# Kernel optimization log

Measured on AMD Instinct MI355X. Metric: run time of the kernel, lower is better.

## Reference

```python
import jax, jax.numpy as jnp
import numpy as np

IN_MODES = (4, 4, 6, 8)  # prod = 768 = d_model; same modes for input and output
D_MODEL = 768
N_HEADS = 12
D_HEAD = D_MODEL // N_HEADS
SCALE = 1.0 / np.sqrt(D_HEAD)
TT_RANKS = (1, 32, 64, 32, 1)


def tt_linear(x, c0, c1, c2, c3, b):
    # TT-factorized linear: cores c_k have shape (r_{k-1}, m_k, n_k, r_k)
    # with in/out modes IN_MODES. x: [B, S, 768]
    B, S, D = x.shape
    t = x.reshape(B * S, *IN_MODES)                     # n i j k l over in-modes
    t = jnp.einsum('nijkl,mir->njklmr', t, c0[0])       # contract n1, r0=1 squeezed
    t = jnp.einsum('njklmr,rpjs->nklmps', t, c1)        # contract n2 and rank r1
    t = jnp.einsum('nklmps,sqkt->nlmpqt', t, c2)        # contract n3 and rank r2
    t = jnp.einsum('nlmpqt,tul->nmpqu', t, c3[..., 0])  # contract n4 and rank r3, r4=1
    return t.reshape(B, S, D) + b                        # out-modes m,p,q,u -> 768


def _make_tt_params(key):
    ks = jax.random.split(key, 4)
    cores = []
    for i in range(4):
        shape = (TT_RANKS[i], IN_MODES[i], IN_MODES[i], TT_RANKS[i + 1])
        cores.append(jax.random.normal(ks[i], shape, jnp.float32) * 0.05)
    bias = jnp.zeros((D_MODEL,), jnp.float32)
    return cores, bias


def setup_inputs() -> dict:
    key = jax.random.key(0)
    kx, kq, kk, kv, ko = jax.random.split(key, 5)
    B, S = 2, 2048
    x = jax.random.normal(kx, (B, S, D_MODEL), jnp.float32)
    mask = jnp.tril(jnp.ones((S, S), dtype=bool))[None, None]  # causal [1,1,S,S]
    out = {'x': x, 'mask': mask}
    for name, k in (('q', kq), ('k', kk), ('v', kv), ('o', ko)):
        cores, bias = _make_tt_params(k)
        for i in range(4):
            out[f'{name}c{i}'] = cores[i]
        out[f'{name}b'] = bias
    return out


def reference(x, mask,
              qc0, qc1, qc2, qc3, qb,
              kc0, kc1, kc2, kc3, kb,
              vc0, vc1, vc2, vc3, vb,
              oc0, oc1, oc2, oc3, ob):
    B, S, _ = x.shape
    q = tt_linear(x, qc0, qc1, qc2, qc3, qb)
    k = tt_linear(x, kc0, kc1, kc2, kc3, kb)
    v = tt_linear(x, vc0, vc1, vc2, vc3, vb)
    # [B, S, H, Dh] -> [B, H, S, Dh]
    q = q.reshape(B, S, N_HEADS, D_HEAD).transpose(0, 2, 1, 3)
    k = k.reshape(B, S, N_HEADS, D_HEAD).transpose(0, 2, 1, 3)
    v = v.reshape(B, S, N_HEADS, D_HEAD).transpose(0, 2, 1, 3)
    scores = jnp.einsum('bhqd,bhkd->bhqk', q, k) * SCALE  # full O(S^2) scores
    scores = jnp.where(mask, scores, jnp.float32(-10000.0))  # masked_fill(mask==0,-1e4)
    attn = jax.nn.softmax(scores, axis=-1)  # dropout is identity at eval
    out = jnp.einsum('bhqk,bhkd->bhqd', attn, v)
    out = out.transpose(0, 2, 1, 3).reshape(B, S, D_MODEL)
    return tt_linear(out, oc0, oc1, oc2, oc3, ob)
```

## Files before the change

kernel.cpp:

```cpp
#include <hip/hip_runtime.h>
#include <cstddef>
#include <cstdint>

#define D_MODEL 768
#define N_HEADS 12
#define SEQ 2048
#define BATCH 2
#define NROWS (BATCH * SEQ)
#define W_ELEMS (D_MODEL * D_MODEL)
#define Y_ELEMS (NROWS * D_MODEL)

typedef __attribute__((ext_vector_type(8))) short bf16x8;
typedef __attribute__((ext_vector_type(4))) float f32x4;

struct TTPtrs {
    const float* c0[4];
    const float* c1[4];
    const float* c2[4];
    const float* c3[4];
};

__device__ __forceinline__ float bf2f(uint16_t u) {
    union { uint32_t u; float f; } c; c.u = ((uint32_t)u) << 16; return c.f;
}
__device__ __forceinline__ uint16_t f2bf(float f) {
    union { float f; uint32_t u; } c; c.f = f;
    uint32_t x = c.u + 0x7fffu + ((c.u >> 16) & 1u);
    return (uint16_t)(x >> 16);
}
__device__ __forceinline__ uint32_t cvtpk(float lo, float hi) {
    uint32_t r;
    asm("v_cvt_pk_bf16_f32 %0, %1, %2" : "=v"(r) : "v"(lo), "v"(hi));
    return r;
}
__device__ __forceinline__ void glds16(const void* g, void* l) {
    auto gp = reinterpret_cast<const __attribute__((address_space(1))) uint32_t*>(
        reinterpret_cast<uintptr_t>(g));
    auto lp = reinterpret_cast<__attribute__((address_space(3))) uint32_t*>(
        reinterpret_cast<uintptr_t>(l));
    __builtin_amdgcn_global_load_lds(gp, lp, 16, 0, 0);
}

__global__ __launch_bounds__(256) void pre_kernel(TTPtrs P, float* __restrict__ wsA,
                                                  const float* __restrict__ x,
                                                  uint16_t* __restrict__ xb) {
    const int bx = blockIdx.x;
    if (bx < 256) {
        const int mat = bx >> 6;
        const float* c0 = P.c0[mat];
        const float* c1 = P.c1[mat];
        float* A = wsA + mat * 16384;
        int idx = (bx & 63) * 256 + threadIdx.x;
        int s = idx & 63, pj = (idx >> 6) & 15, mi = idx >> 10;
        float acc = 0.f;
        #pragma unroll 8
        for (int r = 0; r < 32; r++)
            acc = fmaf(c0[mi * 32 + r], c1[(r * 16 + pj) * 64 + s], acc);
        A[idx] = acc;
    } else {
        int idx = ((bx - 256) * 256 + threadIdx.x) * 4;
        float4 v = *(const float4*)(x + idx);
        *(uint2*)(xb + idx) = make_uint2(cvtpk(v.x, v.y), cvtpk(v.z, v.w));
    }
}

__global__ __launch_bounds__(256) void tt_buildB(TTPtrs P, const float* __restrict__ wsA,
                                                 float* __restrict__ wsB) {
    const int mat = blockIdx.y;
    const float* c2 = P.c2[mat];
    const float* A = wsA + mat * 16384;
    float* B = wsB + (size_t)mat * 294912;
    int idx = blockIdx.x * 256 + threadIdx.x;
    int t = idx & 31;
    int rest = idx >> 5;
    int qk = rest % 36;
    int rest2 = rest / 36;
    int pj = rest2 & 15, mi = rest2 >> 4;
    const float* Arow = A + (mi * 16 + pj) * 64;
    float acc = 0.f;
    #pragma unroll 8
    for (int s = 0; s < 64; s++)
        acc = fmaf(Arow[s], c2[(s * 36 + qk) * 32 + t], acc);
    B[idx] = acc;
}

__global__ __launch_bounds__(256) void tt_buildC(TTPtrs P, const float* __restrict__ wsB,
                                                 uint16_t* __restrict__ Wbf) {
    __shared__ float b_lds[36 * 33];
    __shared__ float c_lds[32 * 64];
    const int mat = blockIdx.y;
    const int mipj = blockIdx.x;
    const int mi = mipj >> 4, pj = mipj & 15;
    const int m = mi >> 2, i = mi & 3, p = pj >> 2, j = pj & 3;
    const float* Bsrc = wsB + (size_t)mat * 294912 + (size_t)mipj * 1152;
    const float* c3 = P.c3[mat];
    uint16_t* Wt = Wbf + (size_t)mat * W_ELEMS;
    const int tid = threadIdx.x;

    for (int e = tid; e < 1152; e += 256) {
        int qk = e >> 5, t = e & 31;
        b_lds[qk * 33 + t] = Bsrc[e];
    }
    for (int e = tid; e < 2048; e += 256)
        c_lds[e] = c3[e];
    __syncthreads();

    const int outbase = (m * 4 + p) * 48;
    const int inbase = (i * 4 + j) * 48;
    #pragma unroll
    for (int n = 0; n < 9; n++) {
        int idx = n * 256 + tid;
        int qu = idx / 48, kl = idx % 48;
        int q = qu >> 3, u = qu & 7, k = kl >> 3, l = kl & 7;
        const float* brow = &b_lds[(q * 6 + k) * 33];
        const float* crow = &c_lds[u * 8 + l];
        float acc = 0.f;
        #pragma unroll 8
        for (int t = 0; t < 32; t++)
            acc = fmaf(brow[t], crow[t * 64], acc);
        Wt[(size_t)(outbase + qu) * D_MODEL + inbase + kl] = f2bf(acc);
    }
}

template <int MODE>
__global__ __launch_bounds__(256) void gemm_mfma(const uint16_t* __restrict__ X,
                                                 const uint16_t* __restrict__ Wall,
                                                 const float* __restrict__ b0,
                                                 const float* __restrict__ b1,
                                                 const float* __restrict__ b2,
                                                 void* __restrict__ Yall,
                                                 uint16_t* __restrict__ Vt) {
    __shared__ uint16_t lds[2][8192];
    const int z = blockIdx.z;
    const uint16_t* W = Wall + (size_t)z * W_ELEMS;
    const float* bias = (z == 0) ? b0 : (z == 1 ? b1 : b2);
    const int m0 = blockIdx.x * 128, n0 = blockIdx.y * 128;
    const int tid = threadIdx.x, w = tid >> 6, l = tid & 63;
    const int wr = w >> 1, wc = w & 1;
    const int l15 = l & 15, lg = l >> 4;

    const int srow = w * 32 + (l >> 2);
    const int scol = ((l & 3) ^ ((l >> 2) & 3)) * 8;
    const uint16_t* Abase = X + (size_t)(m0 + srow) * D_MODEL + scol;
    const uint16_t* Bbase = W + (size_t)(n0 + srow) * D_MODEL + scol;

    f32x4 acc[4][4];
    #pragma unroll
    for (int mi = 0; mi < 4; ++mi)
        #pragma unroll
        for (int ni = 0; ni < 4; ++ni) acc[mi][ni] = (f32x4){0.f, 0.f, 0.f, 0.f};

    auto stage = [&](int buf, int kt) {
        const uint16_t* A0 = Abase + kt * 32;
        const uint16_t* B0 = Bbase + kt * 32;
        glds16(A0, &lds[buf][w * 1024]);
        glds16(A0 + 16 * D_MODEL, &lds[buf][w * 1024 + 512]);
        glds16(B0, &lds[buf][4096 + w * 1024]);
        glds16(B0 + 16 * D_MODEL, &lds[buf][4096 + w * 1024 + 512]);
    };

    stage(0, 0);
    __syncthreads();
    const int roff = ((lg ^ (l & 3)) << 3);
    for (int kt = 0; kt < 24; ++kt) {
        int cur = kt & 1;
        if (kt < 23) stage(cur ^ 1, kt + 1);
        const uint16_t* As = &lds[cur][0];
        const uint16_t* Bs = &lds[cur][4096];
        bf16x8 a[4], bb[4];
        #pragma unroll
        for (int mi = 0; mi < 4; ++mi)
            a[mi] = *(const bf16x8*)(As + (wr * 64 + mi * 16 + l15) * 32 + roff);
        #pragma unroll
        for (int ni = 0; ni < 4; ++ni)
            bb[ni] = *(const bf16x8*)(Bs + (wc * 64 + ni * 16 + l15) * 32 + roff);
        #pragma unroll
        for (int mi = 0; mi < 4; ++mi)
            #pragma unroll
            for (int ni = 0; ni < 4; ++ni)
                acc[mi][ni] = __builtin_amdgcn_mfma_f32_16x16x32_bf16(
                    a[mi], bb[ni], acc[mi][ni], 0, 0, 0);
        __syncthreads();
    }

    float bv[4];
    #pragma unroll
    for (int ni = 0; ni < 4; ++ni) bv[ni] = bias[n0 + wc * 64 + ni * 16 + l15];

    if (MODE == 1 && z == 2) {
        #pragma unroll
        for (int mi = 0; mi < 4; ++mi) {
            int row = m0 + wr * 64 + mi * 16 + lg * 4;
            int bb_ = row >> 11, s = row & 2047;
            #pragma unroll
            for (int ni = 0; ni < 4; ++ni) {
                int col = n0 + wc * 64 + ni * 16 + l15;
                float v0 = acc[mi][ni][0] + bv[ni], v1 = acc[mi][ni][1] + bv[ni];
                float v2 = acc[mi][ni][2] + bv[ni], v3 = acc[mi][ni][3] + bv[ni];
                *(uint2*)(Vt + ((size_t)(bb_ * 12 + (col >> 6)) * 64 + (col & 63)) * 2048 + s) =
                    make_uint2(cvtpk(v0, v1), cvtpk(v2, v3));
            }
        }
    } else {
        #pragma unroll
        for (int mi = 0; mi < 4; ++mi)
            #pragma unroll
            for (int ni = 0; ni < 4; ++ni)
                #pragma unroll
                for (int r = 0; r < 4; ++r) {
                    int row = m0 + wr * 64 + mi * 16 + lg * 4 + r;
                    int col = n0 + wc * 64 + ni * 16 + l15;
                    float v = acc[mi][ni][r] + bv[ni];
                    if (MODE == 1)
                        ((uint16_t*)Yall + (size_t)z * Y_ELEMS)[(size_t)row * D_MODEL + col] = f2bf(v);
                    else
                        ((float*)Yall)[(size_t)row * D_MODEL + col] = v;
                }
    }
}

__global__ __launch_bounds__(256) void attn_mfma(const uint16_t* __restrict__ Q,
                                                 const uint16_t* __restrict__ K,
                                                 const uint16_t* __restrict__ Vt,
                                                 uint16_t* __restrict__ pO1,
                                                 uint16_t* __restrict__ pO2,
                                                 float* __restrict__ tbuf) {
    __shared__ uint16_t ks[2][4096];
    __shared__ uint16_t vs[2][4096];
    __shared__ uint16_t ps[4][1024];

    const int bx = blockIdx.x;
    const int u = bx / 24;
    const int bh = bx % 24;
    int g, c;
    if (u < 32)      { g = u >> 2,            c = u & 3; }
    else if (u < 56) { int t = u - 32; g = 8 + t / 3,  c = t % 3; }
    else if (u < 72) { int t = u - 56; g = 16 + (t >> 1), c = t & 1; }
    else             { g = 24 + (u - 72),     c = 0; }
    const int qt = 31 - g;
    const int ktlo = c * 8;
    const int kthi = min(ktlo + 7, qt);
    const int nkt = kthi - ktlo + 1;

    const int b = bh / 12, h = bh % 12;
    const int tid = threadIdx.x, w = tid >> 6, l = tid & 63;
    const int l15 = l & 15, lg = l >> 4;
    const size_t headoff = (size_t)b * SEQ * D_MODEL + h * 64;
    const size_t vhead = ((size_t)(b * 12 + h)) << 17;
    const int sc8 = ((l & 7) ^ ((l >> 3) & 7)) * 8;
    const int srow = w * 16 + (l >> 3);

    const float QS = 0.125f * 1.44269504088896f;
    bf16x8 qf[2];
    {
        const uint16_t* qp = Q + headoff + (size_t)(qt * 64 + w * 16 + l15) * D_MODEL + lg * 8;
        #pragma unroll
        for (int ds = 0; ds < 2; ++ds) {
            bf16x8 qv = *(const bf16x8*)(qp + ds * 32);
            #pragma unroll
            for (int j = 0; j < 8; ++j)
                qf[ds][j] = (short)f2bf(bf2f((uint16_t)qv[j]) * QS);
        }
    }

    float m_ = -3e38f, l_ = 0.f;
    f32x4 oacc[4];
    #pragma unroll
    for (int ni = 0; ni < 4; ++ni) oacc[ni] = (f32x4){0.f, 0.f, 0.f, 0.f};
    const int qglob = qt * 64 + w * 16 + l15;

    auto stage = [&](int buf, int kt) {
        const uint16_t* ksrc = K + headoff + (size_t)(kt * 64 + srow) * D_MODEL + sc8;
        glds16(ksrc, &ks[buf][w * 1024]);
        glds16(ksrc + 8 * D_MODEL, &ks[buf][w * 1024 + 512]);
        const uint16_t* vsrc = Vt + vhead + (size_t)srow * SEQ + kt * 64 + sc8;
        glds16(vsrc, &vs[buf][w * 1024]);
        glds16(vsrc + 8 * SEQ, &vs[buf][w * 1024 + 512]);
    };

    stage(0, ktlo);
    for (int it = 0; it < nkt; ++it) {
        const int kt = ktlo + it;
        const int cur = it & 1;
        __syncthreads();
        if (it + 1 < nkt) stage(cur ^ 1, kt + 1);

        f32x4 sacc[4];
        #pragma unroll
        for (int ki = 0; ki < 4; ++ki) sacc[ki] = (f32x4){0.f, 0.f, 0.f, 0.f};
        __builtin_amdgcn_s_setprio(1);
        #pragma unroll
        for (int ds = 0; ds < 2; ++ds)
            #pragma unroll
            for (int ki = 0; ki < 4; ++ki) {
                int byte = (ki * 16 + l15) * 128 + ((((ds << 2) + lg) ^ (l15 & 7)) << 4);
                bf16x8 ak = *(const bf16x8*)((const char*)&ks[cur][0] + byte);
                sacc[ki] = __builtin_amdgcn_mfma_f32_16x16x32_bf16(ak, qf[ds], sacc[ki], 0, 0, 0);
            }
        __builtin_amdgcn_s_setprio(0);

        const bool diag = (kt == qt);
        float sv[16];
        #pragma unroll
        for (int ki = 0; ki < 4; ++ki)
            #pragma unroll
            for (int r = 0; r < 4; ++r) {
                float s = sacc[ki][r];
                if (diag) {
                    int key = kt * 64 + ki * 16 + lg * 4 + r;
                    if (key > qglob) s = -3e38f;
                }
                sv[ki * 4 + r] = s;
            }
        float mx = fmaxf(fmaxf(sv[0], sv[1]), sv[2]);
        #pragma unroll
        for (int i = 3; i < 15; i += 2) mx = fmaxf(fmaxf(mx, sv[i]), sv[i + 1]);
        mx = fmaxf(mx, sv[15]);
        mx = fmaxf(mx, __shfl_xor(mx, 16));
        mx = fmaxf(mx, __shfl_xor(mx, 32));
        if (__any(mx > m_ + 11.54f)) {
            float mnew = fmaxf(m_, mx);
            float alpha = __builtin_amdgcn_exp2f(m_ - mnew);
            l_ *= alpha;
            float a0 = __shfl(alpha, lg * 4 + 0), a1 = __shfl(alpha, lg * 4 + 1);
            float a2 = __shfl(alpha, lg * 4 + 2), a3 = __shfl(alpha, lg * 4 + 3);
            #pragma unroll
            for (int ni = 0; ni < 4; ++ni) {
                oacc[ni][0] *= a0; oacc[ni][1] *= a1;
                oacc[ni][2] *= a2; oacc[ni][3] *= a3;
            }
            m_ = mnew;
        }
        float sum = 0.f;
        uint32_t pk[8];
        #pragma unroll
        for (int i = 0; i < 16; i += 2) {
            float p0 = __builtin_amdgcn_exp2f(sv[i] - m_);
            float p1 = __builtin_amdgcn_exp2f(sv[i + 1] - m_);
            sum += p0 + p1;
            pk[i >> 1] = cvtpk(p0, p1);
        }
        sum += __shfl_xor(sum, 16);
        sum += __shfl_xor(sum, 32);
        l_ += sum;

        uint16_t* psw = &ps[w][0];
        #pragma unroll
        for (int ki = 0; ki < 4; ++ki) {
            int byte = (l15 * 128 + ki * 32 + lg * 8) ^ ((l15 & 7) << 4);
            *(uint2*)((char*)psw + byte) = make_uint2(pk[ki * 2], pk[ki * 2 + 1]);
        }
        asm volatile("s_waitcnt lgkmcnt(0)" ::: "memory");
        __builtin_amdgcn_sched_barrier(0);

        __builtin_amdgcn_s_setprio(1);
        #pragma unroll
        for (int kss = 0; kss < 2; ++kss) {
            int pbyte = l15 * 128 + ((((kss << 2) + lg) ^ (l15 & 7)) << 4);
            bf16x8 ap = *(const bf16x8*)((const char*)psw + pbyte);
            #pragma unroll
            for (int ni = 0; ni < 4; ++ni) {
                int vbyte = (ni * 16 + l15) * 128 + ((((kss << 2) + lg) ^ (l15 & 7)) << 4);
                bf16x8 bv = *(const bf16x8*)((const char*)&vs[cur][0] + vbyte);
                oacc[ni] = __builtin_amdgcn_mfma_f32_16x16x32_bf16(ap, bv, oacc[ni], 0, 0, 0);
            }
        }
        __builtin_amdgcn_s_setprio(0);
    }

    float li0 = 1.f / __shfl(l_, lg * 4 + 0), li1 = 1.f / __shfl(l_, lg * 4 + 1);
    float li2 = 1.f / __shfl(l_, lg * 4 + 2), li3 = 1.f / __shfl(l_, lg * 4 + 3);
    uint16_t* op = (bx < 1536) ? (pO1 + (size_t)bx * 4096)
                               : (pO2 + (size_t)(bx - 1536) * 4096);
    #pragma unroll
    for (int ni = 0; ni < 4; ++ni) {
        int col = ni * 16 + l15;
        int rbase = (w * 16 + lg * 4) * 64 + col;
        op[rbase + 0 * 64] = f2bf(oacc[ni][0] * li0);
        op[rbase + 1 * 64] = f2bf(oacc[ni][1] * li1);
        op[rbase + 2 * 64] = f2bf(oacc[ni][2] * li2);
        op[rbase + 3 * 64] = f2bf(oacc[ni][3] * li3);
    }
    if (lg == 0)
        tbuf[(size_t)bx * 64 + w * 16 + l15] = m_ + __log2f(l_);
}

__global__ __launch_bounds__(256) void attn_combine(const uint16_t* __restrict__ pO1,
                                                    const uint16_t* __restrict__ pO2,
                                                    const float* __restrict__ tbuf,
                                                    uint16_t* __restrict__ Obf) {
    __shared__ float t_lds[4][64];
    const int bx = blockIdx.x;
    const int qt = bx & 31, bh = bx >> 5;
    const int b = bh / 12, h = bh % 12;
    const int g = 31 - qt;
    const int u_base = (g < 8) ? 4 * g : (g < 16) ? 32 + 3 * (g - 8)
                     : (g < 24) ? 56 + 2 * (g - 16) : 72 + (g - 24);
    const int nc = (g < 8) ? 4 : (g < 16) ? 3 : (g < 24) ? 2 : 1;
    const int tid = threadIdx.x;
    if (tid < nc * 64) {
        int c = tid >> 6, q = tid & 63;
        t_lds[c][q] = tbuf[(size_t)((u_base + c) * 24 + bh) * 64 + q];
    }
    __syncthreads();

    const int q = tid >> 2, d0 = (tid & 3) * 16;
    float tmax = t_lds[0][q];
    for (int c = 1; c < nc; ++c) tmax = fmaxf(tmax, t_lds[c][q]);
    float acc[16];
    #pragma unroll
    for (int j = 0; j < 16; ++j) acc[j] = 0.f;
    float denom = 0.f;
    for (int c = 0; c < nc; ++c) {
        float wgt = __builtin_amdgcn_exp2f(t_lds[c][q] - tmax);
        denom += wgt;
        int ug = (u_base + c) * 24 + bh;
        const uint16_t* op = (ug < 1536) ? (pO1 + (size_t)ug * 4096)
                                         : (pO2 + (size_t)(ug - 1536) * 4096);
        bf16x8 v0 = *(const bf16x8*)(op + q * 64 + d0);
        bf16x8 v1 = *(const bf16x8*)(op + q * 64 + d0 + 8);
        #pragma unroll
        for (int j = 0; j < 8; ++j) {
            acc[j]     += bf2f((uint16_t)v0[j]) * wgt;
            acc[8 + j] += bf2f((uint16_t)v1[j]) * wgt;
        }
    }
    float inv = 1.f / denom;
    uint32_t outp[8];
    #pragma unroll
    for (int j = 0; j < 8; ++j)
        outp[j] = cvtpk(acc[2 * j] * inv, acc[2 * j + 1] * inv);
    size_t rb = (size_t)(b * SEQ + qt * 64 + q) * D_MODEL + h * 64 + d0;
    *(uint4*)(Obf + rb)     = make_uint4(outp[0], outp[1], outp[2], outp[3]);
    *(uint4*)(Obf + rb + 8) = make_uint4(outp[4], outp[5], outp[6], outp[7]);
}

extern "C" void kernel_launch(void* const* d_in, const int* in_sizes, int n_in,
                              void* d_out, int out_size, void* d_ws, size_t ws_size,
                              hipStream_t stream) {
    const float* x = (const float*)d_in[0];
    TTPtrs P;
    const float* biases[4];
    const int base[4] = {2, 7, 12, 17};
    for (int t = 0; t < 4; t++) {
        P.c0[t] = (const float*)d_in[base[t] + 0];
        P.c1[t] = (const float*)d_in[base[t] + 1];
        P.c2[t] = (const float*)d_in[base[t] + 2];
        P.c3[t] = (const float*)d_in[base[t] + 3];
        biases[t] = (const float*)d_in[base[t] + 4];
    }

    char* ws = (char*)d_ws;
    float* wsA = (float*)(ws + 0);
    float* wsB = (float*)(ws + 262144);
    uint16_t* Wbf = (uint16_t*)(ws + 4980736);
    uint16_t* xbf = (uint16_t*)(ws + 9699328);
    uint16_t* pO2 = (uint16_t*)(ws + 9699328);
    float* tbuf = (float*)(ws + 12845056);
    uint16_t* Qbf = (uint16_t*)(ws + 15990784);
    uint16_t* Kbf = (uint16_t*)(ws + 22282240);
    uint16_t* Vtbf = (uint16_t*)(ws + 28573696);
    uint16_t* Obf = (uint16_t*)(ws + 34865152);
    uint16_t* pO1 = (uint16_t*)d_out;
    (void)Kbf;

    pre_kernel<<<dim3(256 + 3072), 256, 0, stream>>>(P, wsA, x, xbf);
    tt_buildB<<<dim3(1152, 4), 256, 0, stream>>>(P, wsA, wsB);
    tt_buildC<<<dim3(256, 4), 256, 0, stream>>>(P, wsB, Wbf);

    gemm_mfma<1><<<dim3(32, 6, 3), 256, 0, stream>>>(xbf, Wbf, biases[0], biases[1],
                                                     biases[2], (void*)Qbf, Vtbf);
    attn_mfma<<<dim3(1920), 256, 0, stream>>>(Qbf, Kbf, Vtbf, pO1, pO2, tbuf);
    attn_combine<<<dim3(768), 256, 0, stream>>>(pO1, pO2, tbuf, Obf);

    gemm_mfma<0><<<dim3(32, 6, 1), 256, 0, stream>>>(Obf, Wbf + 3 * (size_t)W_ELEMS,
                                                     biases[3], biases[3], biases[3],
                                                     d_out, nullptr);
}
```

Before: 237.5 us.

## Process two query tiles per attention block and stage V transpose through LDS

The attention kernel now handles a 128-row query pair per block, so each K/V tile loaded into LDS is reused by two query tiles. A lookup table reorders the work units and changes the split-K partitioning, and the combine kernel is adapted to the 128-row layout. Separately, the V-transpose epilogue of the QKV GEMM writes through swizzled LDS so that global stores are coalesced 16-byte writes instead of strided 8-byte ones. In exchange, register pressure rises from the doubled accumulators and the grid shrinks to 960 blocks, which may reduce occupancy and load balance.

```diff
diff --git a/kernel.cpp b/kernel.cpp
--- a/kernel.cpp
+++ b/kernel.cpp
@@ -40,6 +40,18 @@
         reinterpret_cast<uintptr_t>(l));
     __builtin_amdgcn_global_load_lds(gp, lp, 16, 0, 0);
 }
+
+__device__ const uint8_t UNITS[40] = {
+    (3<<2)|0,(4<<2)|0,(5<<2)|0,(6<<2)|0,(7<<2)|0,(7<<2)|1,(8<<2)|0,(8<<2)|1,
+    (9<<2)|0,(9<<2)|1,(10<<2)|0,(10<<2)|1,(11<<2)|0,(11<<2)|1,(11<<2)|2,(12<<2)|0,
+    (12<<2)|1,(12<<2)|2,(13<<2)|0,(13<<2)|1,(13<<2)|2,(14<<2)|0,(14<<2)|1,(14<<2)|2,
+    (15<<2)|0,(15<<2)|1,(15<<2)|2,(15<<2)|3,(2<<2)|0,(6<<2)|1,(10<<2)|2,(14<<2)|3,
+    (1<<2)|0,(5<<2)|1,(9<<2)|2,(13<<2)|3,(0<<2)|0,(4<<2)|1,(8<<2)|2,(12<<2)|3};
+__device__ const uint8_t UBASE[64] = {
+    36,0,0,0,  32,0,0,0,  28,0,0,0,  0,0,0,0,
+    1,37,0,0,  2,33,0,0,  3,29,0,0,  4,5,0,0,
+    6,7,38,0,  8,9,34,0,  10,11,30,0, 12,13,14,0,
+    15,16,17,39, 18,19,20,35, 21,22,23,31, 24,25,26,27};
 
 __global__ __launch_bounds__(256) void pre_kernel(TTPtrs P, float* __restrict__ wsA,
                                                   const float* __restrict__ x,
@@ -188,19 +200,38 @@
     for (int ni = 0; ni < 4; ++ni) bv[ni] = bias[n0 + wc * 64 + ni * 16 + l15];
 
     if (MODE == 1 && z == 2) {
+        uint16_t* T = &lds[0][0];
         #pragma unroll
         for (int mi = 0; mi < 4; ++mi) {
-            int row = m0 + wr * 64 + mi * 16 + lg * 4;
-            int bb_ = row >> 11, s = row & 2047;
+            int row = wr * 64 + mi * 16 + lg * 4;
             #pragma unroll
             for (int ni = 0; ni < 4; ++ni) {
-                int col = n0 + wc * 64 + ni * 16 + l15;
+                int col = wc * 64 + ni * 16 + l15;
                 float v0 = acc[mi][ni][0] + bv[ni], v1 = acc[mi][ni][1] + bv[ni];
                 float v2 = acc[mi][ni][2] + bv[ni], v3 = acc[mi][ni][3] + bv[ni];
-                *(uint2*)(Vt + ((size_t)(bb_ * 12 + (col >> 6)) * 64 + (col & 63)) * 2048 + s) =
-                    make_uint2(cvtpk(v0, v1), cvtpk(v2, v3));
-            }
-        }
+                int byte = (col << 8) + (row << 1);
+                byte ^= (((col & 31) ^ (row >> 6)) << 3);
+                *(uint2*)((char*)T + byte) = make_uint2(cvtpk(v0, v1), cvtpk(v2, v3));
+            }
+        }
+        __syncthreads();
+        int col = tid >> 1, half = tid & 1;
+        int gcol = n0 + col;
+        int bb_ = m0 >> 11;
+        int s = (m0 & 2047) + half * 64;
+        uint16_t* dst = Vt + ((size_t)(bb_ * 12 + (gcol >> 6)) * 64 + (gcol & 63)) * 2048 + s;
+        uint2 tv[16];
+        #pragma unroll
+        for (int k = 0; k < 16; ++k) {
+            int r = half * 64 + k * 4;
+            int byte = (col << 8) + (r << 1);
+            byte ^= (((col & 31) ^ (r >> 6)) << 3);
+            tv[k] = *(const uint2*)((const char*)T + byte);
+        }
+        #pragma unroll
+        for (int k = 0; k < 8; ++k)
+            *(uint4*)(dst + k * 8) = make_uint4(tv[2 * k].x, tv[2 * k].y,
+                                                tv[2 * k + 1].x, tv[2 * k + 1].y);
     } else {
         #pragma unroll
         for (int mi = 0; mi < 4; ++mi)
@@ -227,20 +258,14 @@
                                                  float* __restrict__ tbuf) {
     __shared__ uint16_t ks[2][4096];
     __shared__ uint16_t vs[2][4096];
-    __shared__ uint16_t ps[4][1024];
+    __shared__ uint16_t ps[4][2048];
 
     const int bx = blockIdx.x;
-    const int u = bx / 24;
-    const int bh = bx % 24;
-    int g, c;
-    if (u < 32)      { g = u >> 2,            c = u & 3; }
-    else if (u < 56) { int t = u - 32; g = 8 + t / 3,  c = t % 3; }
-    else if (u < 72) { int t = u - 56; g = 16 + (t >> 1), c = t & 1; }
-    else             { g = 24 + (u - 72),     c = 0; }
-    const int qt = 31 - g;
+    const int u = bx / 24, bh = bx % 24;
+    const int jc = UNITS[u];
+    const int j = jc >> 2, c = jc & 3;
     const int ktlo = c * 8;
-    const int kthi = min(ktlo + 7, qt);
-    const int nkt = kthi - ktlo + 1;
+    const int nkt = min(8, 2 * j + 2 - ktlo);
 
     const int b = bh / 12, h = bh % 12;
     const int tid = threadIdx.x, w = tid >> 6, l = tid & 63;
@@ -251,23 +276,30 @@
     const int srow = w * 16 + (l >> 3);
 
     const float QS = 0.125f * 1.44269504088896f;
-    bf16x8 qf[2];
+    bf16x8 qf0[2], qf1[2];
     {
-        const uint16_t* qp = Q + headoff + (size_t)(qt * 64 + w * 16 + l15) * D_MODEL + lg * 8;
+        const uint16_t* qp0 = Q + headoff + (size_t)(j * 128 + w * 16 + l15) * D_MODEL + lg * 8;
+        const uint16_t* qp1 = qp0 + (size_t)64 * D_MODEL;
         #pragma unroll
         for (int ds = 0; ds < 2; ++ds) {
-            bf16x8 qv = *(const bf16x8*)(qp + ds * 32);
-            #pragma unroll
-            for (int j = 0; j < 8; ++j)
-                qf[ds][j] = (short)f2bf(bf2f((uint16_t)qv[j]) * QS);
-        }
-    }
-
-    float m_ = -3e38f, l_ = 0.f;
-    f32x4 oacc[4];
+            bf16x8 a0 = *(const bf16x8*)(qp0 + ds * 32);
+            bf16x8 a1 = *(const bf16x8*)(qp1 + ds * 32);
+            #pragma unroll
+            for (int jj = 0; jj < 8; ++jj) {
+                qf0[ds][jj] = (short)f2bf(bf2f((uint16_t)a0[jj]) * QS);
+                qf1[ds][jj] = (short)f2bf(bf2f((uint16_t)a1[jj]) * QS);
+            }
+        }
+    }
+
+    float m0_ = -3e38f, l0_ = 0.f, m1_ = -3e38f, l1_ = 0.f;
+    f32x4 oacc0[4], oacc1[4];
     #pragma unroll
-    for (int ni = 0; ni < 4; ++ni) oacc[ni] = (f32x4){0.f, 0.f, 0.f, 0.f};
-    const int qglob = qt * 64 + w * 16 + l15;
+    for (int ni = 0; ni < 4; ++ni) {
+        oacc0[ni] = (f32x4){0.f, 0.f, 0.f, 0.f};
+        oacc1[ni] = (f32x4){0.f, 0.f, 0.f, 0.f};
+    }
+    const int qg0 = j * 128 + w * 16 + l15;
 
     auto stage = [&](int buf, int kt) {
         const uint16_t* ksrc = K + headoff + (size_t)(kt * 64 + srow) * D_MODEL + sc8;
@@ -282,73 +314,138 @@
     for (int it = 0; it < nkt; ++it) {
         const int kt = ktlo + it;
         const int cur = it & 1;
+        const bool act0 = (kt <= 2 * j);
         __syncthreads();
         if (it + 1 < nkt) stage(cur ^ 1, kt + 1);
 
-        f32x4 sacc[4];
-        #pragma unroll
-        for (int ki = 0; ki < 4; ++ki) sacc[ki] = (f32x4){0.f, 0.f, 0.f, 0.f};
-        __builtin_amdgcn_s_setprio(1);
+        bf16x8 ak[2][4];
         #pragma unroll
         for (int ds = 0; ds < 2; ++ds)
             #pragma unroll
             for (int ki = 0; ki < 4; ++ki) {
                 int byte = (ki * 16 + l15) * 128 + ((((ds << 2) + lg) ^ (l15 & 7)) << 4);
-                bf16x8 ak = *(const bf16x8*)((const char*)&ks[cur][0] + byte);
-                sacc[ki] = __builtin_amdgcn_mfma_f32_16x16x32_bf16(ak, qf[ds], sacc[ki], 0, 0, 0);
+                ak[ds][ki] = *(const bf16x8*)((const char*)&ks[cur][0] + byte);
+            }
+        f32x4 sacc0[4], sacc1[4];
+        #pragma unroll
+        for (int ki = 0; ki < 4; ++ki) {
+            sacc0[ki] = (f32x4){0.f, 0.f, 0.f, 0.f};
+            sacc1[ki] = (f32x4){0.f, 0.f, 0.f, 0.f};
+        }
+        __builtin_amdgcn_s_setprio(1);
+        #pragma unroll
+        for (int ds = 0; ds < 2; ++ds)
+            #pragma unroll
+            for (int ki = 0; ki < 4; ++ki) {
+                if (act0)
+                    sacc0[ki] = __builtin_amdgcn_mfma_f32_16x16x32_bf16(ak[ds][ki], qf0[ds], sacc0[ki], 0, 0, 0);
+                sacc1[ki] = __builtin_amdgcn_mfma_f32_16x16x32_bf16(ak[ds][ki], qf1[ds], sacc1[ki], 0, 0, 0);
             }
         __builtin_amdgcn_s_setprio(0);
 
-        const bool diag = (kt == qt);
-        float sv[16];
-        #pragma unroll
-        for (int ki = 0; ki < 4; ++ki)
-            #pragma unroll
-            for (int r = 0; r < 4; ++r) {
-                float s = sacc[ki][r];
-                if (diag) {
-                    int key = kt * 64 + ki * 16 + lg * 4 + r;
-                    if (key > qglob) s = -3e38f;
+        if (act0) {
+            const bool diag = (kt == 2 * j);
+            float sv[16];
+            #pragma unroll
+            for (int ki = 0; ki < 4; ++ki)
+                #pragma unroll
+                for (int r = 0; r < 4; ++r) {
+                    float s = sacc0[ki][r];
+                    if (diag) {
+                        int key = kt * 64 + ki * 16 + lg * 4 + r;
+                        if (key > qg0) s = -3e38f;
+                    }
+                    sv[ki * 4 + r] = s;
                 }
-                sv[ki * 4 + r] = s;
-            }
-        float mx = fmaxf(fmaxf(sv[0], sv[1]), sv[2]);
-        #pragma unroll
-        for (int i = 3; i < 15; i += 2) mx = fmaxf(fmaxf(mx, sv[i]), sv[i + 1]);
-        mx = fmaxf(mx, sv[15]);
-        mx = fmaxf(mx, __shfl_xor(mx, 16));
-        mx = fmaxf(mx, __shfl_xor(mx, 32));
-        if (__any(mx > m_ + 11.54f)) {
-            float mnew = fmaxf(m_, mx);
-            float alpha = __builtin_amdgcn_exp2f(m_ - mnew);
-            l_ *= alpha;
-            float a0 = __shfl(alpha, lg * 4 + 0), a1 = __shfl(alpha, lg * 4 + 1);
-            float a2 = __shfl(alpha, lg * 4 + 2), a3 = __shfl(alpha, lg * 4 + 3);
-            #pragma unroll
-            for (int ni = 0; ni < 4; ++ni) {
-                oacc[ni][0] *= a0; oacc[ni][1] *= a1;
-                oacc[ni][2] *= a2; oacc[ni][3] *= a3;
-            }
-            m_ = mnew;
-        }
-        float sum = 0.f;
-        uint32_t pk[8];
-        #pragma unroll
-        for (int i = 0; i < 16; i += 2) {
-            float p0 = __builtin_amdgcn_exp2f(sv[i] - m_);
-            float p1 = __builtin_amdgcn_exp2f(sv[i + 1] - m_);
-            sum += p0 + p1;
-            pk[i >> 1] = cvtpk(p0, p1);
-        }
-        sum += __shfl_xor(sum, 16);
-        sum += __shfl_xor(sum, 32);
-        l_ += sum;
-
-        uint16_t* psw = &ps[w][0];
-        #pragma unroll
-        for (int ki = 0; ki < 4; ++ki) {
-            int byte = (l15 * 128 + ki * 32 + lg * 8) ^ ((l15 & 7) << 4);
-            *(uint2*)((char*)psw + byte) = make_uint2(pk[ki * 2], pk[ki * 2 + 1]);
+            float mx = fmaxf(fmaxf(sv[0], sv[1]), sv[2]);
+            #pragma unroll
+            for (int i = 3; i < 15; i += 2) mx = fmaxf(fmaxf(mx, sv[i]), sv[i + 1]);
+            mx = fmaxf(mx, sv[15]);
+            mx = fmaxf(mx, __shfl_xor(mx, 16));
+            mx = fmaxf(mx, __shfl_xor(mx, 32));
+            if (__any(mx > m0_ + 11.54f)) {
+                float mnew = fmaxf(m0_, mx);
+                float alpha = __builtin_amdgcn_exp2f(m0_ - mnew);
+                l0_ *= alpha;
+                float a0 = __shfl(alpha, lg * 4 + 0), a1 = __shfl(alpha, lg * 4 + 1);
+                float a2 = __shfl(alpha, lg * 4 + 2), a3 = __shfl(alpha, lg * 4 + 3);
+                #pragma unroll
+                for (int ni = 0; ni < 4; ++ni) {
+                    oacc0[ni][0] *= a0; oacc0[ni][1] *= a1;
+                    oacc0[ni][2] *= a2; oacc0[ni][3] *= a3;
+                }
+                m0_ = mnew;
+            }
+            float sum = 0.f;
+            uint32_t pk[8];
+            #pragma unroll
+            for (int i = 0; i < 16; i += 2) {
+                float p0 = __builtin_amdgcn_exp2f(sv[i] - m0_);
+                float p1 = __builtin_amdgcn_exp2f(sv[i + 1] - m0_);
+                sum += p0 + p1;
+                pk[i >> 1] = cvtpk(p0, p1);
+            }
+            sum += __shfl_xor(sum, 16);
+            sum += __shfl_xor(sum, 32);
+            l0_ += sum;
+            char* psw = (char*)&ps[w][0];
+            #pragma unroll
+            for (int ki = 0; ki < 4; ++ki) {
+                int byte = (l15 * 128 + ki * 32 + lg * 8) ^ ((l15 & 7) << 4);
+                *(uint2*)(psw + byte) = make_uint2(pk[ki * 2], pk[ki * 2 + 1]);
+            }
+        }
+        {
+            const bool diag = (kt == 2 * j + 1);
+            float sv[16];
+            #pragma unroll
+            for (int ki = 0; ki < 4; ++ki)
+                #pragma unroll
+                for (int r = 0; r < 4; ++r) {
+                    float s = sacc1[ki][r];
+                    if (diag) {
+                        int key = kt * 64 + ki * 16 + lg * 4 + r;
+                        if (key > qg0 + 64) s = -3e38f;
+                    }
+                    sv[ki * 4 + r] = s;
+                }
+            float mx = fmaxf(fmaxf(sv[0], sv[1]), sv[2]);
+            #pragma unroll
+            for (int i = 3; i < 15; i += 2) mx = fmaxf(fmaxf(mx, sv[i]), sv[i + 1]);
+            mx = fmaxf(mx, sv[15]);
+            mx = fmaxf(mx, __shfl_xor(mx, 16));
+            mx = fmaxf(mx, __shfl_xor(mx, 32));
+            if (__any(mx > m1_ + 11.54f)) {
+                float mnew = fmaxf(m1_, mx);
+                float alpha = __builtin_amdgcn_exp2f(m1_ - mnew);
+                l1_ *= alpha;
+                float a0 = __shfl(alpha, lg * 4 + 0), a1 = __shfl(alpha, lg * 4 + 1);
+                float a2 = __shfl(alpha, lg * 4 + 2), a3 = __shfl(alpha, lg * 4 + 3);
+                #pragma unroll
+                for (int ni = 0; ni < 4; ++ni) {
+                    oacc1[ni][0] *= a0; oacc1[ni][1] *= a1;
+                    oacc1[ni][2] *= a2; oacc1[ni][3] *= a3;
+                }
+                m1_ = mnew;
+            }
+            float sum = 0.f;
+            uint32_t pk[8];
+            #pragma unroll
+            for (int i = 0; i < 16; i += 2) {
+                float p0 = __builtin_amdgcn_exp2f(sv[i] - m1_);
+                float p1 = __builtin_amdgcn_exp2f(sv[i + 1] - m1_);
+                sum += p0 + p1;
+                pk[i >> 1] = cvtpk(p0, p1);
+            }
+            sum += __shfl_xor(sum, 16);
+            sum += __shfl_xor(sum, 32);
+            l1_ += sum;
+            char* psw = (char*)&ps[w][1024];
+            #pragma unroll
+            for (int ki = 0; ki < 4; ++ki) {
+                int byte = (l15 * 128 + ki * 32 + lg * 8) ^ ((l15 & 7) << 4);
+                *(uint2*)(psw + byte) = make_uint2(pk[ki * 2], pk[ki * 2 + 1]);
+            }
         }
         asm volatile("s_waitcnt lgkmcnt(0)" ::: "memory");
         __builtin_amdgcn_sched_barrier(0);
@@ -357,82 +454,100 @@
         #pragma unroll
         for (int kss = 0; kss < 2; ++kss) {
             int pbyte = l15 * 128 + ((((kss << 2) + lg) ^ (l15 & 7)) << 4);
-            bf16x8 ap = *(const bf16x8*)((const char*)psw + pbyte);
+            bf16x8 ap0 = *(const bf16x8*)((const char*)&ps[w][0] + pbyte);
+            bf16x8 ap1 = *(const bf16x8*)((const char*)&ps[w][1024] + pbyte);
             #pragma unroll
             for (int ni = 0; ni < 4; ++ni) {
                 int vbyte = (ni * 16 + l15) * 128 + ((((kss << 2) + lg) ^ (l15 & 7)) << 4);
-                bf16x8 bv = *(const bf16x8*)((const char*)&vs[cur][0] + vbyte);
-                oacc[ni] = __builtin_amdgcn_mfma_f32_16x16x32_bf16(ap, bv, oacc[ni], 0, 0, 0);
+                bf16x8 bvv = *(const bf16x8*)((const char*)&vs[cur][0] + vbyte);
+                if (act0)
+                    oacc0[ni] = __builtin_amdgcn_mfma_f32_16x16x32_bf16(ap0, bvv, oacc0[ni], 0, 0, 0);
+                oacc1[ni] = __builtin_amdgcn_mfma_f32_16x16x32_bf16(ap1, bvv, oacc1[ni], 0, 0, 0);
             }
         }
         __builtin_amdgcn_s_setprio(0);
     }
 
-    float li0 = 1.f / __shfl(l_, lg * 4 + 0), li1 = 1.f / __shfl(l_, lg * 4 + 1);
-    float li2 = 1.f / __shfl(l_, lg * 4 + 2), li3 = 1.f / __shfl(l_, lg * 4 + 3);
-    uint16_t* op = (bx < 1536) ? (pO1 + (size_t)bx * 4096)
-                               : (pO2 + (size_t)(bx - 1536) * 4096);
-    #pragma unroll
-    for (int ni = 0; ni < 4; ++ni) {
-        int col = ni * 16 + l15;
-        int rbase = (w * 16 + lg * 4) * 64 + col;
-        op[rbase + 0 * 64] = f2bf(oacc[ni][0] * li0);
-        op[rbase + 1 * 64] = f2bf(oacc[ni][1] * li1);
-        op[rbase + 2 * 64] = f2bf(oacc[ni][2] * li2);
-        op[rbase + 3 * 64] = f2bf(oacc[ni][3] * li3);
-    }
-    if (lg == 0)
-        tbuf[(size_t)bx * 64 + w * 16 + l15] = m_ + __log2f(l_);
+    uint16_t* op = (bx < 768) ? (pO1 + (size_t)bx * 8192)
+                              : (pO2 + (size_t)(bx - 768) * 8192);
+    {
+        float li0 = 1.f / __shfl(l0_, lg * 4 + 0), li1 = 1.f / __shfl(l0_, lg * 4 + 1);
+        float li2 = 1.f / __shfl(l0_, lg * 4 + 2), li3 = 1.f / __shfl(l0_, lg * 4 + 3);
+        #pragma unroll
+        for (int ni = 0; ni < 4; ++ni) {
+            int rbase = (w * 16 + lg * 4) * 64 + ni * 16 + l15;
+            op[rbase + 0 * 64] = f2bf(oacc0[ni][0] * li0);
+            op[rbase + 1 * 64] = f2bf(oacc0[ni][1] * li1);
+            op[rbase + 2 * 64] = f2bf(oacc0[ni][2] * li2);
+            op[rbase + 3 * 64] = f2bf(oacc0[ni][3] * li3);
+        }
+    }
+    {
+        float li0 = 1.f / __shfl(l1_, lg * 4 + 0), li1 = 1.f / __shfl(l1_, lg * 4 + 1);
+        float li2 = 1.f / __shfl(l1_, lg * 4 + 2), li3 = 1.f / __shfl(l1_, lg * 4 + 3);
+        #pragma unroll
+        for (int ni = 0; ni < 4; ++ni) {
+            int rbase = (64 + w * 16 + lg * 4) * 64 + ni * 16 + l15;
+            op[rbase + 0 * 64] = f2bf(oacc1[ni][0] * li0);
+            op[rbase + 1 * 64] = f2bf(oacc1[ni][1] * li1);
+            op[rbase + 2 * 64] = f2bf(oacc1[ni][2] * li2);
+            op[rbase + 3 * 64] = f2bf(oacc1[ni][3] * li3);
+        }
+    }
+    if (lg == 0) {
+        tbuf[(size_t)bx * 128 + w * 16 + l15] = m0_ + __log2f(l0_);
+        tbuf[(size_t)bx * 128 + 64 + w * 16 + l15] = m1_ + __log2f(l1_);
+    }
 }
 
 __global__ __launch_bounds__(256) void attn_combine(const uint16_t* __restrict__ pO1,
                                                     const uint16_t* __restrict__ pO2,
                                                     const float* __restrict__ tbuf,
                                                     uint16_t* __restrict__ Obf) {
-    __shared__ float t_lds[4][64];
+    __shared__ float t_lds[4][128];
     const int bx = blockIdx.x;
-    const int qt = bx & 31, bh = bx >> 5;
+    const int j = bx & 15, bh = bx >> 4;
     const int b = bh / 12, h = bh % 12;
-    const int g = 31 - qt;
-    const int u_base = (g < 8) ? 4 * g : (g < 16) ? 32 + 3 * (g - 8)
-                     : (g < 24) ? 56 + 2 * (g - 16) : 72 + (g - 24);
-    const int nc = (g < 8) ? 4 : (g < 16) ? 3 : (g < 24) ? 2 : 1;
+    const int nc = (j < 4) ? 1 : (j < 8) ? 2 : (j < 12) ? 3 : 4;
     const int tid = threadIdx.x;
-    if (tid < nc * 64) {
-        int c = tid >> 6, q = tid & 63;
-        t_lds[c][q] = tbuf[(size_t)((u_base + c) * 24 + bh) * 64 + q];
+    for (int e = tid; e < nc * 128; e += 256) {
+        int cc = e >> 7, q = e & 127;
+        int ug = UBASE[j * 4 + cc] * 24 + bh;
+        t_lds[cc][q] = tbuf[(size_t)ug * 128 + q];
     }
     __syncthreads();
 
-    const int q = tid >> 2, d0 = (tid & 3) * 16;
+    const int q = tid >> 1, d0 = (tid & 1) * 32;
     float tmax = t_lds[0][q];
     for (int c = 1; c < nc; ++c) tmax = fmaxf(tmax, t_lds[c][q]);
-    float acc[16];
+    float acc[32];
     #pragma unroll
-    for (int j = 0; j < 16; ++j) acc[j] = 0.f;
+    for (int jj = 0; jj < 32; ++jj) acc[jj] = 0.f;
     float denom = 0.f;
     for (int c = 0; c < nc; ++c) {
         float wgt = __builtin_amdgcn_exp2f(t_lds[c][q] - tmax);
         denom += wgt;
-        int ug = (u_base + c) * 24 + bh;
-        const uint16_t* op = (ug < 1536) ? (pO1 + (size_t)ug * 4096)
-                                         : (pO2 + (size_t)(ug - 1536) * 4096);
-        bf16x8 v0 = *(const bf16x8*)(op + q * 64 + d0);
-        bf16x8 v1 = *(const bf16x8*)(op + q * 64 + d0 + 8);
-        #pragma unroll
-        for (int j = 0; j < 8; ++j) {
-            acc[j]     += bf2f((uint16_t)v0[j]) * wgt;
-            acc[8 + j] += bf2f((uint16_t)v1[j]) * wgt;
+        int ug = UBASE[j * 4 + c] * 24 + bh;
+        const uint16_t* op = (ug < 768) ? (pO1 + (size_t)ug * 8192)
+                                        : (pO2 + (size_t)(ug - 768) * 8192);
+        #pragma unroll
+        for (int v = 0; v < 4; ++v) {
+            bf16x8 vv = *(const bf16x8*)(op + q * 64 + d0 + v * 8);
+            #pragma unroll
+            for (int jj = 0; jj < 8; ++jj)
+                acc[v * 8 + jj] += bf2f((uint16_t)vv[jj]) * wgt;
         }
     }
     float inv = 1.f / denom;
-    uint32_t outp[8];
+    uint32_t outp[16];
     #pragma unroll
-    for (int j = 0; j < 8; ++j)
-        outp[j] = cvtpk(acc[2 * j] * inv, acc[2 * j + 1] * inv);
-    size_t rb = (size_t)(b * SEQ + qt * 64 + q) * D_MODEL + h * 64 + d0;
-    *(uint4*)(Obf + rb)     = make_uint4(outp[0], outp[1], outp[2], outp[3]);
-    *(uint4*)(Obf + rb + 8) = make_uint4(outp[4], outp[5], outp[6], outp[7]);
+    for (int jj = 0; jj < 16; ++jj)
+        outp[jj] = cvtpk(acc[2 * jj] * inv, acc[2 * jj + 1] * inv);
+    size_t rb = (size_t)(b * SEQ + j * 128 + q) * D_MODEL + h * 64 + d0;
+    *(uint4*)(Obf + rb)      = make_uint4(outp[0], outp[1], outp[2], outp[3]);
+    *(uint4*)(Obf + rb + 8)  = make_uint4(outp[4], outp[5], outp[6], outp[7]);
+    *(uint4*)(Obf + rb + 16) = make_uint4(outp[8], outp[9], outp[10], outp[11]);
+    *(uint4*)(Obf + rb + 24) = make_uint4(outp[12], outp[13], outp[14], outp[15]);
 }
 
 extern "C" void kernel_launch(void* const* d_in, const int* in_sizes, int n_in,
@@ -470,8 +585,8 @@
 
     gemm_mfma<1><<<dim3(32, 6, 3), 256, 0, stream>>>(xbf, Wbf, biases[0], biases[1],
                                                      biases[2], (void*)Qbf, Vtbf);
-    attn_mfma<<<dim3(1920), 256, 0, stream>>>(Qbf, Kbf, Vtbf, pO1, pO2, tbuf);
-    attn_combine<<<dim3(768), 256, 0, stream>>>(pO1, pO2, tbuf, Obf);
+    attn_mfma<<<dim3(960), 256, 0, stream>>>(Qbf, Kbf, Vtbf, pO1, pO2, tbuf);
+    attn_combine<<<dim3(384), 256, 0, stream>>>(pO1, pO2, tbuf, Obf);
 
     gemm_mfma<0><<<dim3(32, 6, 1), 256, 0, stream>>>(Obf, Wbf + 3 * (size_t)W_ELEMS,
                                                      biases[3], biases[3], biases[3],
```

Result: slower. 261.1 us (+10.0%).
